# Kernel optimization log

Hardware: AMD Instinct MI355X
Metric: run time of the kernel (lower is better)

Reference implementation:

```python
import jax, jax.numpy as jnp
import numpy as np

N_NODES = 100000
N_EDGES = 1600000
C_IN = 128
C_HID = 128
C_OUT = 128


def _gcn_conv(x, row, col, ew, W, b, n_nodes):
    # PyG GCNConv with edge weights and self-loops already included in (row, col, ew).
    # deg[i] = sum of edge weights into node i (flow source->target, aggregate at col)
    xw = x @ W                                                # [N, C_out]
    deg = jax.ops.segment_sum(ew, col, num_segments=n_nodes)  # [N]
    dinv = jnp.where(deg > 0, jax.lax.rsqrt(deg), 0.0)        # deg^{-1/2}, inf -> 0
    norm = dinv[row] * ew * dinv[col]                         # [E]
    msg = xw[row] * norm[:, None]                             # gather + scale
    out = jax.ops.segment_sum(msg, col, num_segments=n_nodes) # scatter-add
    return out + b


def setup_inputs() -> dict:
    key = jax.random.key(0)
    ks = jax.random.split(key, 10)
    x = jax.random.normal(ks[0], (N_NODES, C_IN), dtype=jnp.float32)
    edge_index = jax.random.randint(ks[1], (2, N_EDGES), 0, N_NODES, dtype=jnp.int32)
    edge_weight = jax.random.uniform(ks[2], (N_EDGES,), dtype=jnp.float32)
    s = 1.0 / np.sqrt(C_HID)
    W1 = jax.random.uniform(ks[3], (C_IN, C_HID), minval=-s, maxval=s, dtype=jnp.float32)
    b1 = jnp.zeros((C_HID,), dtype=jnp.float32)
    W2 = jax.random.uniform(ks[4], (C_HID, C_HID), minval=-s, maxval=s, dtype=jnp.float32)
    b2 = jnp.zeros((C_HID,), dtype=jnp.float32)
    W3 = jax.random.uniform(ks[5], (C_HID, C_OUT), minval=-s, maxval=s, dtype=jnp.float32)
    b3 = jnp.zeros((C_OUT,), dtype=jnp.float32)
    return {"x": x, "edge_index": edge_index, "edge_weight": edge_weight,
            "W1": W1, "b1": b1, "W2": W2, "b2": b2, "W3": W3, "b3": b3}


def reference(x, edge_index, edge_weight, W1, b1, W2, b2, W3, b3):
    n = x.shape[0]
    # add self-loops with weight 1 (PyG add_self_loops; identical each layer, built once)
    loop = jnp.arange(n, dtype=edge_index.dtype)
    row = jnp.concatenate([edge_index[0], loop])
    col = jnp.concatenate([edge_index[1], loop])
    ew = jnp.concatenate([edge_weight, jnp.ones((n,), dtype=edge_weight.dtype)])
    h = _gcn_conv(x, row, col, ew, W1, b1, n)
    h = jax.nn.relu(h)
    h = _gcn_conv(h, row, col, ew, W2, b2, n)
    h = jax.nn.relu(h)
    h = _gcn_conv(h, row, col, ew, W3, b3, n)
    return h
```

## Files before the change

### kernel.cpp

```cpp
#include <hip/hip_runtime.h>

#define NN 100000
#define NE 1600000

static __device__ __forceinline__ unsigned f2bf_rne(float f) {
    unsigned u = __float_as_uint(f);
    return (u + 0x7FFFu + ((u >> 16) & 1u)) >> 16;
}
static __device__ __forceinline__ float bf_lo(unsigned u) { return __uint_as_float(u << 16); }
static __device__ __forceinline__ float bf_hi(unsigned u) { return __uint_as_float(u & 0xFFFF0000u); }

__global__ __launch_bounds__(256) void k_init(unsigned long long* packed, int n) {
    int i = blockIdx.x * 256 + threadIdx.x;
    if (i < n) packed[i] = 0ull;
}

template <typename STORE>
static __device__ __forceinline__ void gemm_core(const float* __restrict__ W,
                                                 float* sW, const float* sA,
                                                 int t, size_t r0, STORE&& store) {
    int rr = (t >> 5) << 2;
    int cc = (t & 31) << 2;
    float acc[4][4] = {{0.0f}};
    const float4* W4 = (const float4*)W;
    float4* sW4 = (float4*)sW;

    for (int kc = 0; kc < 128; kc += 32) {
#pragma unroll
        for (int i = 0; i < 4; ++i) sW4[t + 256 * i] = W4[(kc * 32) + t + 256 * i];
        __syncthreads();
#pragma unroll 2
        for (int k = 0; k < 32; k += 4) {
            float4 w0 = *(const float4*)&sW[(k + 0) * 128 + cc];
            float4 w1 = *(const float4*)&sW[(k + 1) * 128 + cc];
            float4 w2 = *(const float4*)&sW[(k + 2) * 128 + cc];
            float4 w3 = *(const float4*)&sW[(k + 3) * 128 + cc];
#pragma unroll
            for (int i = 0; i < 4; ++i) {
                float4 a = *(const float4*)&sA[(rr + i) * 128 + kc + k];
                acc[i][0] = fmaf(a.x, w0.x, acc[i][0]);
                acc[i][1] = fmaf(a.x, w0.y, acc[i][1]);
                acc[i][2] = fmaf(a.x, w0.z, acc[i][2]);
                acc[i][3] = fmaf(a.x, w0.w, acc[i][3]);
                acc[i][0] = fmaf(a.y, w1.x, acc[i][0]);
                acc[i][1] = fmaf(a.y, w1.y, acc[i][1]);
                acc[i][2] = fmaf(a.y, w1.z, acc[i][2]);
                acc[i][3] = fmaf(a.y, w1.w, acc[i][3]);
                acc[i][0] = fmaf(a.z, w2.x, acc[i][0]);
                acc[i][1] = fmaf(a.z, w2.y, acc[i][1]);
                acc[i][2] = fmaf(a.z, w2.z, acc[i][2]);
                acc[i][3] = fmaf(a.z, w2.w, acc[i][3]);
                acc[i][0] = fmaf(a.w, w3.x, acc[i][0]);
                acc[i][1] = fmaf(a.w, w3.y, acc[i][1]);
                acc[i][2] = fmaf(a.w, w3.z, acc[i][2]);
                acc[i][3] = fmaf(a.w, w3.w, acc[i][3]);
            }
        }
        __syncthreads();
    }
    store(rr, cc, acc);
}

__global__ __launch_bounds__(256) void k_gp(const float* __restrict__ A,
                                            const float* __restrict__ W,
                                            unsigned* __restrict__ Cb,
                                            const int* __restrict__ col,
                                            const float* __restrict__ ew,
                                            unsigned long long* packed,
                                            int* __restrict__ rank, int e) {
    __shared__ float sW[32 * 128];
    __shared__ float sA[32 * 128];
    int b = blockIdx.x;
    int sub = b % 3;
    int q = b / 3;
    int t = threadIdx.x;

    if (sub != 0) {
        int p = q * 2 + sub - 1;
        int i = p * 256 + t;
        if (i < e) {
            int c = col[i];
            unsigned fe = (unsigned)__float2uint_rn(ew[i] * 1048576.0f);
            unsigned long long inc = ((unsigned long long)fe << 24) | 1ull;
            unsigned long long old = atomicAdd(&packed[c], inc);
            rank[i] = (int)(old & 0xFFFFFFull);
        }
        return;
    }

    size_t r0 = (size_t)q * 32;
    const float4* A4 = (const float4*)(A + r0 * 128);
    float4* sA4 = (float4*)sA;
#pragma unroll
    for (int i = 0; i < 4; ++i) sA4[t + 256 * i] = A4[t + 256 * i];

    gemm_core(W, sW, sA, t, r0, [&](int rr, int cc, float acc[4][4]) {
#pragma unroll
        for (int i = 0; i < 4; ++i) {
            unsigned lo = f2bf_rne(acc[i][0]) | (f2bf_rne(acc[i][1]) << 16);
            unsigned hi = f2bf_rne(acc[i][2]) | (f2bf_rne(acc[i][3]) << 16);
            *(uint2*)&Cb[((r0 + rr + i) * 128 + cc) >> 1] = make_uint2(lo, hi);
        }
    });
}

__global__ __launch_bounds__(256) void k_scan1(const unsigned long long* __restrict__ packed,
                                               int* __restrict__ rowptr,
                                               int* __restrict__ part,
                                               float* __restrict__ dinv, int n) {
    __shared__ int s[256];
    int t = threadIdx.x;
    int i = blockIdx.x * 256 + t;
    unsigned long long pk = (i < n) ? packed[i] : 0ull;
    int v = (int)(pk & 0xFFFFFFull);
    if (i < n) {
        float deg = 1.0f + (float)(pk >> 24) * (1.0f / 1048576.0f);
        dinv[i] = rsqrtf(deg);
    }
    s[t] = v;
    __syncthreads();
    for (int d = 1; d < 256; d <<= 1) {
        int y = (t >= d) ? s[t - d] : 0;
        __syncthreads();
        s[t] += y;
        __syncthreads();
    }
    if (i < n) rowptr[i] = s[t] - v;
    if (t == 255) part[blockIdx.x] = s[255];
}

__global__ __launch_bounds__(512) void k_scan2(int* part, int m) {
    __shared__ int s[512];
    int t = threadIdx.x;
    int v = (t < m) ? part[t] : 0;
    s[t] = v;
    __syncthreads();
    for (int d = 1; d < 512; d <<= 1) {
        int y = (t >= d) ? s[t - d] : 0;
        __syncthreads();
        s[t] += y;
        __syncthreads();
    }
    if (t < m) part[t] = s[t] - v;
}

__global__ __launch_bounds__(256) void k_scan3(int* rowptr, const int* __restrict__ part, int n, int e) {
    int i = blockIdx.x * 256 + threadIdx.x;
    if (i < n) rowptr[i] += part[blockIdx.x];
    if (i == 0) rowptr[n] = e;
}

__global__ __launch_bounds__(256) void k_fill(const int* __restrict__ row,
                                              const int* __restrict__ col,
                                              const float* __restrict__ ew,
                                              const int* __restrict__ rowptr,
                                              const int* __restrict__ rank,
                                              const float* __restrict__ dinv,
                                              uint2* __restrict__ meta, int e) {
    int i = blockIdx.x * 256 + threadIdx.x;
    if (i < e) {
        int c = col[i];
        int r = row[i];
        int p = rowptr[c] + rank[i];
        float w = dinv[r] * ew[i] * dinv[c];
        meta[p] = make_uint2((unsigned)r, __float_as_uint(w));
    }
}

__global__ __launch_bounds__(256) void k_gemm_b(const unsigned* __restrict__ Ab,
                                                const float* __restrict__ W,
                                                unsigned* __restrict__ Cb) {
    __shared__ float sW[32 * 128];
    __shared__ float sA[32 * 128];
    int t = threadIdx.x;
    size_t r0 = (size_t)blockIdx.x * 32;

    const uint2* A2 = (const uint2*)(Ab + r0 * 64);
#pragma unroll
    for (int i = 0; i < 4; ++i) {
        int j = t + 256 * i;
        uint2 u = A2[j];
        float4 f = make_float4(bf_lo(u.x), bf_hi(u.x), bf_lo(u.y), bf_hi(u.y));
        *(float4*)&sA[4 * j] = f;
    }

    gemm_core(W, sW, sA, t, r0, [&](int rr, int cc, float acc[4][4]) {
#pragma unroll
        for (int i = 0; i < 4; ++i) {
            unsigned lo = f2bf_rne(acc[i][0]) | (f2bf_rne(acc[i][1]) << 16);
            unsigned hi = f2bf_rne(acc[i][2]) | (f2bf_rne(acc[i][3]) << 16);
            *(uint2*)&Cb[((r0 + rr + i) * 128 + cc) >> 1] = make_uint2(lo, hi);
        }
    });
}

__global__ __launch_bounds__(256) void k_agg(const unsigned* __restrict__ XWb,
                                             const int* __restrict__ rowptr,
                                             const uint2* __restrict__ meta,
                                             const float* __restrict__ dinv,
                                             const float* __restrict__ bias,
                                             unsigned* __restrict__ outb,
                                             float* __restrict__ outf, int relu, int n) {
    int lane = threadIdx.x & 63;
    int node = blockIdx.x * 4 + (threadIdx.x >> 6);
    if (node >= n) return;

    float di = dinv[node];
    float selfw = di * di;
    unsigned uself = XWb[(size_t)node * 64 + lane];
    float2 bv = *(const float2*)(bias + lane * 2);
    float ax = fmaf(selfw, bf_lo(uself), bv.x);
    float ay = fmaf(selfw, bf_hi(uself), bv.y);

    int p0 = rowptr[node], p1 = rowptr[node + 1];
    for (int base = p0; base < p1; base += 64) {
        int m = p1 - base; if (m > 64) m = 64;
        int idx = base + (lane < m ? lane : m - 1);
        uint2 mv = meta[idx];
        int sv = (int)mv.x;
        float wv = __uint_as_float(mv.y);
        int j = 0;
        for (; j + 8 <= m; j += 8) {
            int s0 = __shfl(sv, j),     s1 = __shfl(sv, j + 1);
            int s2 = __shfl(sv, j + 2), s3 = __shfl(sv, j + 3);
            int s4 = __shfl(sv, j + 4), s5 = __shfl(sv, j + 5);
            int s6 = __shfl(sv, j + 6), s7 = __shfl(sv, j + 7);
            float w0 = __shfl(wv, j),     w1 = __shfl(wv, j + 1);
            float w2 = __shfl(wv, j + 2), w3 = __shfl(wv, j + 3);
            float w4 = __shfl(wv, j + 4), w5 = __shfl(wv, j + 5);
            float w6 = __shfl(wv, j + 6), w7 = __shfl(wv, j + 7);
            unsigned u0 = XWb[(size_t)s0 * 64 + lane];
            unsigned u1 = XWb[(size_t)s1 * 64 + lane];
            unsigned u2 = XWb[(size_t)s2 * 64 + lane];
            unsigned u3 = XWb[(size_t)s3 * 64 + lane];
            unsigned u4 = XWb[(size_t)s4 * 64 + lane];
            unsigned u5 = XWb[(size_t)s5 * 64 + lane];
            unsigned u6 = XWb[(size_t)s6 * 64 + lane];
            unsigned u7 = XWb[(size_t)s7 * 64 + lane];
            ax = fmaf(w0, bf_lo(u0), ax);  ay = fmaf(w0, bf_hi(u0), ay);
            ax = fmaf(w1, bf_lo(u1), ax);  ay = fmaf(w1, bf_hi(u1), ay);
            ax = fmaf(w2, bf_lo(u2), ax);  ay = fmaf(w2, bf_hi(u2), ay);
            ax = fmaf(w3, bf_lo(u3), ax);  ay = fmaf(w3, bf_hi(u3), ay);
            ax = fmaf(w4, bf_lo(u4), ax);  ay = fmaf(w4, bf_hi(u4), ay);
            ax = fmaf(w5, bf_lo(u5), ax);  ay = fmaf(w5, bf_hi(u5), ay);
            ax = fmaf(w6, bf_lo(u6), ax);  ay = fmaf(w6, bf_hi(u6), ay);
            ax = fmaf(w7, bf_lo(u7), ax);  ay = fmaf(w7, bf_hi(u7), ay);
        }
        for (; j + 4 <= m; j += 4) {
            int s0 = __shfl(sv, j),     s1 = __shfl(sv, j + 1);
            int s2 = __shfl(sv, j + 2), s3 = __shfl(sv, j + 3);
            float w0 = __shfl(wv, j),     w1 = __shfl(wv, j + 1);
            float w2 = __shfl(wv, j + 2), w3 = __shfl(wv, j + 3);
            unsigned u0 = XWb[(size_t)s0 * 64 + lane];
            unsigned u1 = XWb[(size_t)s1 * 64 + lane];
            unsigned u2 = XWb[(size_t)s2 * 64 + lane];
            unsigned u3 = XWb[(size_t)s3 * 64 + lane];
            ax = fmaf(w0, bf_lo(u0), ax);  ay = fmaf(w0, bf_hi(u0), ay);
            ax = fmaf(w1, bf_lo(u1), ax);  ay = fmaf(w1, bf_hi(u1), ay);
            ax = fmaf(w2, bf_lo(u2), ax);  ay = fmaf(w2, bf_hi(u2), ay);
            ax = fmaf(w3, bf_lo(u3), ax);  ay = fmaf(w3, bf_hi(u3), ay);
        }
        for (; j < m; ++j) {
            int s = __shfl(sv, j);
            float w = __shfl(wv, j);
            unsigned u = XWb[(size_t)s * 64 + lane];
            ax = fmaf(w, bf_lo(u), ax);
            ay = fmaf(w, bf_hi(u), ay);
        }
    }
    if (relu) {
        ax = fmaxf(ax, 0.0f);
        ay = fmaxf(ay, 0.0f);
        outb[(size_t)node * 64 + lane] = f2bf_rne(ax) | (f2bf_rne(ay) << 16);
    } else {
        *(float2*)(outf + (size_t)node * 128 + lane * 2) = make_float2(ax, ay);
    }
}

extern "C" void kernel_launch(void* const* d_in, const int* in_sizes, int n_in,
                              void* d_out, int out_size, void* d_ws, size_t ws_size,
                              hipStream_t stream) {
    const float* x  = (const float*)d_in[0];
    const int*   ei = (const int*)d_in[1];
    const float* ew = (const float*)d_in[2];
    const float* W1 = (const float*)d_in[3];
    const float* b1 = (const float*)d_in[4];
    const float* W2 = (const float*)d_in[5];
    const float* b2 = (const float*)d_in[6];
    const float* W3 = (const float*)d_in[7];
    const float* b3 = (const float*)d_in[8];
    float* out = (float*)d_out;

    const int n = NN, e = NE;
    const int* row = ei;
    const int* col = ei + e;

    char* ws = (char*)d_ws;
    size_t off = 0;
    auto alloc = [&](size_t bytes) -> void* {
        void* p = ws + off;
        off = (off + bytes + 255) & ~(size_t)255;
        return p;
    };
    unsigned*           hb     = (unsigned*)          alloc((size_t)n * 128 * 2);
    unsigned*           xwb    = (unsigned*)          alloc((size_t)n * 128 * 2);
    unsigned long long* packed = (unsigned long long*)alloc((size_t)n * 8);
    float*              dinv   = (float*)             alloc((size_t)n * 4);
    int*                rowptr = (int*)               alloc((size_t)(n + 1) * 4);
    int*                rank   = (int*)               alloc((size_t)e * 4);
    uint2*              meta   = (uint2*)             alloc((size_t)e * 8);
    int*                part   = (int*)               alloc(512 * 4);
    (void)ws_size; (void)in_sizes; (void)n_in; (void)out_size;

    int nb = (n + 255) / 256;
    int eb = (e + 255) / 256;
    int gb = n / 32;
    int ab = (n + 3) / 4;

    k_init<<<nb, 256, 0, stream>>>(packed, n);
    k_gp<<<gb + eb, 256, 0, stream>>>(x, W1, xwb, col, ew, packed, rank, e);
    k_scan1<<<nb, 256, 0, stream>>>(packed, rowptr, part, dinv, n);
    k_scan2<<<1, 512, 0, stream>>>(part, nb);
    k_scan3<<<nb, 256, 0, stream>>>(rowptr, part, n, e);
    k_fill<<<eb, 256, 0, stream>>>(row, col, ew, rowptr, rank, dinv, meta, e);

    k_agg<<<ab, 256, 0, stream>>>(xwb, rowptr, meta, dinv, b1, hb, (float*)nullptr, 1, n);
    k_gemm_b<<<gb, 256, 0, stream>>>(hb, W2, xwb);
    k_agg<<<ab, 256, 0, stream>>>(xwb, rowptr, meta, dinv, b2, hb, (float*)nullptr, 1, n);
    k_gemm_b<<<gb, 256, 0, stream>>>(hb, W3, xwb);
    k_agg<<<ab, 256, 0, stream>>>(xwb, rowptr, meta, dinv, b3, (unsigned*)nullptr, out, 0, n);
}
```

Measured before the change: 523.7 us.

## Replace FP32 SIMT GEMMs with split-bf16 MFMA tiles and pre-transposed weights

```diff
diff --git a/kernel.cpp b/kernel.cpp
--- a/kernel.cpp
+++ b/kernel.cpp
@@ -2,6 +2,9 @@
 
 #define NN 100000
 #define NE 1600000
+
+typedef __attribute__((ext_vector_type(8))) short short8;
+typedef __attribute__((ext_vector_type(4))) float f32x4;
 
 static __device__ __forceinline__ unsigned f2bf_rne(float f) {
     unsigned u = __float_as_uint(f);
@@ -15,61 +18,91 @@
     if (i < n) packed[i] = 0ull;
 }
 
-template <typename STORE>
-static __device__ __forceinline__ void gemm_core(const float* __restrict__ W,
-                                                 float* sW, const float* sA,
-                                                 int t, size_t r0, STORE&& store) {
-    int rr = (t >> 5) << 2;
-    int cc = (t & 31) << 2;
-    float acc[4][4] = {{0.0f}};
-    const float4* W4 = (const float4*)W;
-    float4* sW4 = (float4*)sW;
-
-    for (int kc = 0; kc < 128; kc += 32) {
-#pragma unroll
-        for (int i = 0; i < 4; ++i) sW4[t + 256 * i] = W4[(kc * 32) + t + 256 * i];
-        __syncthreads();
-#pragma unroll 2
-        for (int k = 0; k < 32; k += 4) {
-            float4 w0 = *(const float4*)&sW[(k + 0) * 128 + cc];
-            float4 w1 = *(const float4*)&sW[(k + 1) * 128 + cc];
-            float4 w2 = *(const float4*)&sW[(k + 2) * 128 + cc];
-            float4 w3 = *(const float4*)&sW[(k + 3) * 128 + cc];
-#pragma unroll
-            for (int i = 0; i < 4; ++i) {
-                float4 a = *(const float4*)&sA[(rr + i) * 128 + kc + k];
-                acc[i][0] = fmaf(a.x, w0.x, acc[i][0]);
-                acc[i][1] = fmaf(a.x, w0.y, acc[i][1]);
-                acc[i][2] = fmaf(a.x, w0.z, acc[i][2]);
-                acc[i][3] = fmaf(a.x, w0.w, acc[i][3]);
-                acc[i][0] = fmaf(a.y, w1.x, acc[i][0]);
-                acc[i][1] = fmaf(a.y, w1.y, acc[i][1]);
-                acc[i][2] = fmaf(a.y, w1.z, acc[i][2]);
-                acc[i][3] = fmaf(a.y, w1.w, acc[i][3]);
-                acc[i][0] = fmaf(a.z, w2.x, acc[i][0]);
-                acc[i][1] = fmaf(a.z, w2.y, acc[i][1]);
-                acc[i][2] = fmaf(a.z, w2.z, acc[i][2]);
-                acc[i][3] = fmaf(a.z, w2.w, acc[i][3]);
-                acc[i][0] = fmaf(a.w, w3.x, acc[i][0]);
-                acc[i][1] = fmaf(a.w, w3.y, acc[i][1]);
-                acc[i][2] = fmaf(a.w, w3.z, acc[i][2]);
-                acc[i][3] = fmaf(a.w, w3.w, acc[i][3]);
+__global__ __launch_bounds__(256) void k_prep(const float* __restrict__ W,
+                                              ushort* __restrict__ Wth,
+                                              ushort* __restrict__ Wtl) {
+    int idx = blockIdx.x * 256 + threadIdx.x;
+    int k = idx >> 7, n = idx & 127;
+    float w = W[idx];
+    unsigned hi = f2bf_rne(w);
+    unsigned lo = f2bf_rne(w - bf_lo(hi));
+    Wth[n * 128 + k] = (ushort)hi;
+    Wtl[n * 128 + k] = (ushort)lo;
+}
+
+template <bool SPLIT_A>
+static __device__ __forceinline__ void mfma_tile(const ushort* sAh, const ushort* sAl,
+                                                 const ushort* __restrict__ Wth,
+                                                 const ushort* __restrict__ Wtl,
+                                                 unsigned* __restrict__ Cb,
+                                                 size_t r0, int t) {
+    int w  = t >> 6;
+    int l  = t & 63;
+    int lr = l & 15;
+    int lk = (l >> 4) << 3;
+    int n0 = w * 32;
+
+    short8 bh[2][4], bl[2][4];
+#pragma unroll
+    for (int cf = 0; cf < 2; ++cf)
+#pragma unroll
+        for (int ks = 0; ks < 4; ++ks) {
+            int n = n0 + cf * 16 + lr;
+            bh[cf][ks] = *(const short8*)&Wth[n * 128 + ks * 32 + lk];
+            bl[cf][ks] = *(const short8*)&Wtl[n * 128 + ks * 32 + lk];
+        }
+
+    f32x4 zero = {0.f, 0.f, 0.f, 0.f};
+    f32x4 acc[2][2] = {{zero, zero}, {zero, zero}};
+
+    __syncthreads();
+
+#pragma unroll
+    for (int ks = 0; ks < 4; ++ks) {
+        short8 ah[2], al[2];
+#pragma unroll
+        for (int rf = 0; rf < 2; ++rf) {
+            int off = (rf * 16 + lr) * 136 + ks * 32 + lk;
+            ah[rf] = *(const short8*)&sAh[off];
+            if (SPLIT_A) al[rf] = *(const short8*)&sAl[off];
+        }
+#pragma unroll
+        for (int rf = 0; rf < 2; ++rf)
+#pragma unroll
+            for (int cf = 0; cf < 2; ++cf) {
+                acc[rf][cf] = __builtin_amdgcn_mfma_f32_16x16x32_bf16(ah[rf], bh[cf][ks], acc[rf][cf], 0, 0, 0);
+                acc[rf][cf] = __builtin_amdgcn_mfma_f32_16x16x32_bf16(ah[rf], bl[cf][ks], acc[rf][cf], 0, 0, 0);
+                if (SPLIT_A)
+                    acc[rf][cf] = __builtin_amdgcn_mfma_f32_16x16x32_bf16(al[rf], bh[cf][ks], acc[rf][cf], 0, 0, 0);
             }
-        }
-        __syncthreads();
-    }
-    store(rr, cc, acc);
+    }
+
+#pragma unroll
+    for (int rf = 0; rf < 2; ++rf)
+#pragma unroll
+        for (int cf = 0; cf < 2; ++cf)
+#pragma unroll
+            for (int r = 0; r < 4; ++r) {
+                unsigned b = f2bf_rne(acc[rf][cf][r]);
+                unsigned p = (unsigned)__shfl_xor((int)b, 1);
+                if (!(l & 1)) {
+                    size_t row = r0 + rf * 16 + ((l >> 4) << 2) + r;
+                    int c = n0 + cf * 16 + lr;
+                    Cb[(row * 128 + c) >> 1] = b | (p << 16);
+                }
+            }
 }
 
 __global__ __launch_bounds__(256) void k_gp(const float* __restrict__ A,
-                                            const float* __restrict__ W,
+                                            const ushort* __restrict__ Wth,
+                                            const ushort* __restrict__ Wtl,
                                             unsigned* __restrict__ Cb,
                                             const int* __restrict__ col,
                                             const float* __restrict__ ew,
                                             unsigned long long* packed,
                                             int* __restrict__ rank, int e) {
-    __shared__ float sW[32 * 128];
-    __shared__ float sA[32 * 128];
+    __shared__ alignas(16) ushort sAh[32 * 136];
+    __shared__ alignas(16) ushort sAl[32 * 136];
     int b = blockIdx.x;
     int sub = b % 3;
     int q = b / 3;
@@ -90,18 +123,19 @@
 
     size_t r0 = (size_t)q * 32;
     const float4* A4 = (const float4*)(A + r0 * 128);
-    float4* sA4 = (float4*)sA;
-#pragma unroll
-    for (int i = 0; i < 4; ++i) sA4[t + 256 * i] = A4[t + 256 * i];
-
-    gemm_core(W, sW, sA, t, r0, [&](int rr, int cc, float acc[4][4]) {
-#pragma unroll
-        for (int i = 0; i < 4; ++i) {
-            unsigned lo = f2bf_rne(acc[i][0]) | (f2bf_rne(acc[i][1]) << 16);
-            unsigned hi = f2bf_rne(acc[i][2]) | (f2bf_rne(acc[i][3]) << 16);
-            *(uint2*)&Cb[((r0 + rr + i) * 128 + cc) >> 1] = make_uint2(lo, hi);
-        }
-    });
+#pragma unroll
+    for (int i = 0; i < 4; ++i) {
+        int j = t + 256 * i;
+        float4 f = A4[j];
+        int rr = j >> 5;
+        int cc = (j & 31) << 2;
+        unsigned h0 = f2bf_rne(f.x), h1 = f2bf_rne(f.y), h2 = f2bf_rne(f.z), h3 = f2bf_rne(f.w);
+        unsigned g0 = f2bf_rne(f.x - bf_lo(h0)), g1 = f2bf_rne(f.y - bf_lo(h1));
+        unsigned g2 = f2bf_rne(f.z - bf_lo(h2)), g3 = f2bf_rne(f.w - bf_lo(h3));
+        *(ushort4*)&sAh[rr * 136 + cc] = make_ushort4((ushort)h0, (ushort)h1, (ushort)h2, (ushort)h3);
+        *(ushort4*)&sAl[rr * 136 + cc] = make_ushort4((ushort)g0, (ushort)g1, (ushort)g2, (ushort)g3);
+    }
+    mfma_tile<true>(sAh, sAl, Wth, Wtl, Cb, r0, t);
 }
 
 __global__ __launch_bounds__(256) void k_scan1(const unsigned long long* __restrict__ packed,
@@ -168,30 +202,23 @@
 }
 
 __global__ __launch_bounds__(256) void k_gemm_b(const unsigned* __restrict__ Ab,
-                                                const float* __restrict__ W,
+                                                const ushort* __restrict__ Wth,
+                                                const ushort* __restrict__ Wtl,
                                                 unsigned* __restrict__ Cb) {
-    __shared__ float sW[32 * 128];
-    __shared__ float sA[32 * 128];
+    __shared__ alignas(16) ushort sA[32 * 136];
     int t = threadIdx.x;
     size_t r0 = (size_t)blockIdx.x * 32;
 
-    const uint2* A2 = (const uint2*)(Ab + r0 * 64);
-#pragma unroll
-    for (int i = 0; i < 4; ++i) {
+    const uint4* A4 = (const uint4*)(Ab + r0 * 64);
+#pragma unroll
+    for (int i = 0; i < 2; ++i) {
         int j = t + 256 * i;
-        uint2 u = A2[j];
-        float4 f = make_float4(bf_lo(u.x), bf_hi(u.x), bf_lo(u.y), bf_hi(u.y));
-        *(float4*)&sA[4 * j] = f;
-    }
-
-    gemm_core(W, sW, sA, t, r0, [&](int rr, int cc, float acc[4][4]) {
-#pragma unroll
-        for (int i = 0; i < 4; ++i) {
-            unsigned lo = f2bf_rne(acc[i][0]) | (f2bf_rne(acc[i][1]) << 16);
-            unsigned hi = f2bf_rne(acc[i][2]) | (f2bf_rne(acc[i][3]) << 16);
-            *(uint2*)&Cb[((r0 + rr + i) * 128 + cc) >> 1] = make_uint2(lo, hi);
-        }
-    });
+        uint4 u = A4[j];
+        int rr = j >> 4;
+        int cc = (j & 15) << 3;
+        *(uint4*)&sA[rr * 136 + cc] = u;
+    }
+    mfma_tile<false>(sA, nullptr, Wth, Wtl, Cb, r0, t);
 }
 
 __global__ __launch_bounds__(256) void k_agg(const unsigned* __restrict__ XWb,
@@ -310,6 +337,7 @@
     int*                rank   = (int*)               alloc((size_t)e * 4);
     uint2*              meta   = (uint2*)             alloc((size_t)e * 8);
     int*                part   = (int*)               alloc(512 * 4);
+    ushort*             wt     = (ushort*)            alloc(6 * 16384 * 2);
     (void)ws_size; (void)in_sizes; (void)n_in; (void)out_size;
 
     int nb = (n + 255) / 256;
@@ -318,15 +346,19 @@
     int ab = (n + 3) / 4;
 
     k_init<<<nb, 256, 0, stream>>>(packed, n);
-    k_gp<<<gb + eb, 256, 0, stream>>>(x, W1, xwb, col, ew, packed, rank, e);
+    k_prep<<<64, 256, 0, stream>>>(W1, wt + 0 * 16384, wt + 1 * 16384);
+    k_prep<<<64, 256, 0, stream>>>(W2, wt + 2 * 16384, wt + 3 * 16384);
+    k_prep<<<64, 256, 0, stream>>>(W3, wt + 4 * 16384, wt + 5 * 16384);
+
+    k_gp<<<gb + eb, 256, 0, stream>>>(x, wt + 0 * 16384, wt + 1 * 16384, xwb, col, ew, packed, rank, e);
     k_scan1<<<nb, 256, 0, stream>>>(packed, rowptr, part, dinv, n);
     k_scan2<<<1, 512, 0, stream>>>(part, nb);
     k_scan3<<<nb, 256, 0, stream>>>(rowptr, part, n, e);
     k_fill<<<eb, 256, 0, stream>>>(row, col, ew, rowptr, rank, dinv, meta, e);
 
     k_agg<<<ab, 256, 0, stream>>>(xwb, rowptr, meta, dinv, b1, hb, (float*)nullptr, 1, n);
-    k_gemm_b<<<gb, 256, 0, stream>>>(hb, W2, xwb);
+    k_gemm_b<<<gb, 256, 0, stream>>>(hb, wt + 2 * 16384, wt + 3 * 16384, xwb);
     k_agg<<<ab, 256, 0, stream>>>(xwb, rowptr, meta, dinv, b2, hb, (float*)nullptr, 1, n);
-    k_gemm_b<<<gb, 256, 0, stream>>>(hb, W3, xwb);
+    k_gemm_b<<<gb, 256, 0, stream>>>(hb, wt + 4 * 16384, wt + 5 * 16384, xwb);
     k_agg<<<ab, 256, 0, stream>>>(xwb, rowptr, meta, dinv, b3, (unsigned*)nullptr, out, 0, n);
 }
```

New measurement: 491.5 us. 1.07x faster.
